# Performance work log

Hardware: AMD Instinct MI355X
Metric: run time of the kernel (lower is better)

The kernel has to match this reference:

```python
import jax, jax.numpy as jnp
import numpy as np

N = 100_000      # nodes
E = 1_600_000    # edges
C_IN = 3         # pos dim
C = 128          # inter_dim == oup_dim
EPS = 1e-5       # BatchNorm eps


def setup_inputs() -> dict:
    key = jax.random.key(0)
    ks = iter(jax.random.split(key, 64))
    inp = {}
    inp['pos'] = jax.random.normal(next(ks), (N, C_IN), dtype=jnp.float32)
    inp['edge_index'] = jax.random.randint(next(ks), (2, E), 0, N, dtype=jnp.int32)
    dims = [C_IN, C, C, C, C]
    for i in range(1, 5):
        cin, cout = dims[i - 1], dims[i]
        inp[f'wl{i}'] = jax.random.normal(next(ks), (cin, cout), jnp.float32) * 0.05
        inp[f'bl{i}'] = jnp.zeros((cout,), jnp.float32)
        inp[f'wr{i}'] = jax.random.normal(next(ks), (cin, cout), jnp.float32) * 0.05
        inp[f'g{i}'] = jax.random.uniform(next(ks), (cout,), jnp.float32, 0.5, 1.5)
        inp[f'be{i}'] = jax.random.normal(next(ks), (cout,), jnp.float32) * 0.1
        inp[f'm{i}'] = jax.random.normal(next(ks), (cout,), jnp.float32) * 0.1
        inp[f'v{i}'] = jax.random.uniform(next(ks), (cout,), jnp.float32, 0.5, 1.5)
    for j, (cin, cout) in enumerate([(C, C), (C, C), (C, C)], start=1):
        inp[f'wf{j}'] = jax.random.normal(next(ks), (cin, cout), jnp.float32) * 0.05
        inp[f'bf{j}'] = jnp.zeros((cout,), jnp.float32)
    return inp


def _sage(x, src, dst, wl, bl, wr):
    # PyG SAGEConv: lin_l(mean_{j->i} x_j) + lin_r(x_i)
    msg_sum = jax.ops.segment_sum(x[src], dst, num_segments=N)          # [N, Cin]
    deg = jax.ops.segment_sum(jnp.ones((src.shape[0], 1), x.dtype), dst, num_segments=N)
    agg = msg_sum / jnp.maximum(deg, 1.0)
    return agg @ wl + bl + x @ wr


def _bn(x, g, b, m, v):
    return g * (x - m) * jax.lax.rsqrt(v + EPS) + b


def reference(pos, edge_index,
              wl1, bl1, wr1, g1, be1, m1, v1,
              wl2, bl2, wr2, g2, be2, m2, v2,
              wl3, bl3, wr3, g3, be3, m3, v3,
              wl4, bl4, wr4, g4, be4, m4, v4,
              wf1, bf1, wf2, bf2, wf3, bf3):
    src, dst = edge_index[0], edge_index[1]
    layers = [(wl1, bl1, wr1, g1, be1, m1, v1),
              (wl2, bl2, wr2, g2, be2, m2, v2),
              (wl3, bl3, wr3, g3, be3, m3, v3),
              (wl4, bl4, wr4, g4, be4, m4, v4)]
    x = pos
    for (wl, bl, wr, g, b, m, v) in layers:
        x = jax.nn.relu(_bn(_sage(x, src, dst, wl, bl, wr), g, b, m, v))
        # dropout p=0.1 inactive at inference
    x = x @ wf1 + bf1
    x = jax.nn.relu(x) @ wf2 + bf2
    x = x @ wf3 + bf3
    return x  # cls=False: raw output, no log_softmax
```

## Files before the change

kernel.cpp:

```cpp
#include <hip/hip_runtime.h>

#define NN 100000
#define EE 1600000
#define CC 128
#define NP 100032
#define NBK 782
#define BCAP 2304

typedef _Float16 f16;
typedef __attribute__((ext_vector_type(2))) f16 f16x2;
typedef __attribute__((ext_vector_type(8))) f16 f16x8;
typedef __attribute__((ext_vector_type(4))) float f32x4;

#define MFMA16(a, b, c) __builtin_amdgcn_mfma_f32_16x16x32_f16(a, b, c, 0, 0, 0)

__global__ __launch_bounds__(1024) void k_part(const int* __restrict__ src,
                                               const int* __restrict__ dst,
                                               int* __restrict__ bcur,
                                               unsigned* __restrict__ bedge) {
  __shared__ int hist[NBK];
  __shared__ int base[NBK];
  const int t = threadIdx.x;
  for (int i = t; i < NBK; i += 1024) hist[i] = 0;
  __syncthreads();
  const int4* src4 = (const int4*)src;
  const int4* dst4 = (const int4*)dst;
  int4 s[4], d[4];
  int rk[16];
  bool val[4];
#pragma unroll
  for (int w = 0; w < 4; w++) {
    int i4 = blockIdx.x * 4096 + w * 1024 + t;
    val[w] = (i4 < EE / 4);
    if (val[w]) {
      s[w] = src4[i4];
      d[w] = dst4[i4];
      rk[w * 4 + 0] = atomicAdd(&hist[d[w].x >> 7], 1);
      rk[w * 4 + 1] = atomicAdd(&hist[d[w].y >> 7], 1);
      rk[w * 4 + 2] = atomicAdd(&hist[d[w].z >> 7], 1);
      rk[w * 4 + 3] = atomicAdd(&hist[d[w].w >> 7], 1);
    }
  }
  __syncthreads();
  for (int i = t; i < NBK; i += 1024) {
    int c = hist[i];
    base[i] = c ? atomicAdd(&bcur[i], c) : 0;
  }
  __syncthreads();
#pragma unroll
  for (int w = 0; w < 4; w++) {
    if (val[w]) {
      int ss[4] = {s[w].x, s[w].y, s[w].z, s[w].w};
      int dd[4] = {d[w].x, d[w].y, d[w].z, d[w].w};
#pragma unroll
      for (int q = 0; q < 4; q++) {
        int b = dd[q] >> 7;
        int slot = base[b] + rk[w * 4 + q];
        if (slot < BCAP)
          bedge[(size_t)b * BCAP + slot] =
              (unsigned)ss[q] | ((unsigned)(dd[q] & 127) << 17);
      }
    }
  }
}

__global__ __launch_bounds__(1024) void k_bscan(const int* __restrict__ bcur,
                                                int* __restrict__ bbase,
                                                int* __restrict__ off) {
  __shared__ int sh[1024];
  int t = threadIdx.x;
  int v = (t < NBK) ? min(bcur[t], BCAP) : 0;
  sh[t] = v;
  __syncthreads();
  for (int d = 1; d < 1024; d <<= 1) {
    int a = (t >= d) ? sh[t - d] : 0;
    __syncthreads();
    sh[t] += a;
    __syncthreads();
  }
  if (t < NBK) bbase[t] = sh[t] - v;
  if (t == 1023) off[NN] = sh[1023];
}

__global__ __launch_bounds__(256) void k_bfill2(const int* __restrict__ bcur,
                                                const int* __restrict__ bbase,
                                                const unsigned* __restrict__ bedge,
                                                int* __restrict__ off,
                                                int* __restrict__ csr) {
  __shared__ int h[128];
  __shared__ int sc[128];
  __shared__ int curs[128];
  const int b = blockIdx.x;
  const int t = threadIdx.x;
  if (t < 128) h[t] = 0;
  __syncthreads();
  const int cnt = min(bcur[b], BCAP);
  const unsigned* be = bedge + (size_t)b * BCAP;
  for (int i = t; i < cnt; i += 256) atomicAdd(&h[(be[i] >> 17) & 127], 1);
  __syncthreads();
  int v = (t < 128) ? h[t] : 0;
  if (t < 128) sc[t] = v;
  __syncthreads();
  for (int d = 1; d < 128; d <<= 1) {
    int a = (t >= d && t < 128) ? sc[t - d] : 0;
    __syncthreads();
    if (t < 128) sc[t] += a;
    __syncthreads();
  }
  if (t < 128) {
    int o = bbase[b] + sc[t] - v;
    int n = b * 128 + t;
    if (n < NN) off[n] = o;
    curs[t] = o;
  }
  __syncthreads();
  for (int i = t; i < cnt; i += 256) {
    unsigned u = be[i];
    int node = (u >> 17) & 127;
    int p = atomicAdd(&curs[node], 1);
    csr[p] = (int)(u & 0x1FFFF);
  }
}

struct WPtrs { const float* w[9]; };
__global__ __launch_bounds__(256) void k_packw(WPtrs wp, f16* __restrict__ out) {
  int t = blockIdx.x * 256 + threadIdx.x;
  int mat = t >> 14;
  int idx = t & 16383;
  int j = idx & 7;
  int lane = (idx >> 3) & 63;
  int ks = (idx >> 9) & 3;
  int nt = idx >> 11;
  int c16 = lane & 15, quad = lane >> 4;
  int k = ks * 32 + quad * 8 + j;
  int n = nt * 16 + c16;
  out[(size_t)mat * 16384 + idx] = (f16)wp.w[mat][k * CC + n];
}

__global__ __launch_bounds__(256) void k_agg3(const int* __restrict__ off,
                                              const int* __restrict__ csr,
                                              const float* __restrict__ pos,
                                              float* __restrict__ agg3) {
  int n = blockIdx.x * 256 + threadIdx.x;
  if (n >= NN) return;
  int b = off[n], e = off[n + 1];
  float a0 = 0.f, a1 = 0.f, a2 = 0.f;
  int i = b;
  for (; i + 4 <= e; i += 4) {
    int s0 = csr[i], s1 = csr[i + 1], s2 = csr[i + 2], s3 = csr[i + 3];
    float p00 = pos[s0 * 3 + 0], p01 = pos[s0 * 3 + 1], p02 = pos[s0 * 3 + 2];
    float p10 = pos[s1 * 3 + 0], p11 = pos[s1 * 3 + 1], p12 = pos[s1 * 3 + 2];
    float p20 = pos[s2 * 3 + 0], p21 = pos[s2 * 3 + 1], p22 = pos[s2 * 3 + 2];
    float p30 = pos[s3 * 3 + 0], p31 = pos[s3 * 3 + 1], p32 = pos[s3 * 3 + 2];
    a0 += (p00 + p10) + (p20 + p30);
    a1 += (p01 + p11) + (p21 + p31);
    a2 += (p02 + p12) + (p22 + p32);
  }
  for (; i < e; i++) {
    int s = csr[i];
    a0 += pos[s * 3 + 0];
    a1 += pos[s * 3 + 1];
    a2 += pos[s * 3 + 2];
  }
  float rd = 1.0f / fmaxf((float)(e - b), 1.0f);
  agg3[n * 3 + 0] = a0 * rd;
  agg3[n * 3 + 1] = a1 * rd;
  agg3[n * 3 + 2] = a2 * rd;
}

__global__ __launch_bounds__(256) void k_node1(
    const float* __restrict__ agg3, const float* __restrict__ pos,
    const float* __restrict__ wl, const float* __restrict__ bl,
    const float* __restrict__ wr, const float* __restrict__ g,
    const float* __restrict__ be, const float* __restrict__ bm,
    const float* __restrict__ bv, f16* __restrict__ x) {
  const int c = threadIdx.x & 127;
  const int np = threadIdx.x >> 7;
  const float Wl0 = wl[c], Wl1 = wl[CC + c], Wl2 = wl[2 * CC + c];
  const float Wr0 = wr[c], Wr1 = wr[CC + c], Wr2 = wr[2 * CC + c];
  const float sc = g[c] * rsqrtf(bv[c] + 1e-5f);
  const float o0 = be[c] + (bl[c] - bm[c]) * sc;
  const int nbase = blockIdx.x * 256;
  const int nend = min(nbase + 256, NN);
#pragma unroll 4
  for (int n = nbase + np; n < nend; n += 2) {
    float acc = agg3[n * 3 + 0] * Wl0 + agg3[n * 3 + 1] * Wl1 +
                agg3[n * 3 + 2] * Wl2 + pos[n * 3 + 0] * Wr0 +
                pos[n * 3 + 1] * Wr1 + pos[n * 3 + 2] * Wr2;
    x[(size_t)n * CC + c] = (f16)fmaxf(acc * sc + o0, 0.0f);
  }
}

__global__ __launch_bounds__(256) void k_aggregate(const int* __restrict__ off,
                                                   const int* __restrict__ csr,
                                                   const f16* __restrict__ x,
                                                   f16* __restrict__ agg) {
  const int n = blockIdx.x * 4 + (threadIdx.x >> 6);
  const int lane = threadIdx.x & 63;
  const int b = off[n], e = off[n + 1];
  float a0 = 0.f, a1 = 0.f;
  int i = b;
  for (; i + 16 <= e; i += 16) {
    int sdx[16];
#pragma unroll
    for (int q = 0; q < 16; q++) sdx[q] = csr[i + q];
    f16x2 v[16];
#pragma unroll
    for (int q = 0; q < 16; q++)
      v[q] = *(const f16x2*)(x + (size_t)sdx[q] * CC + lane * 2);
#pragma unroll
    for (int q = 0; q < 16; q++) {
      a0 += (float)v[q][0];
      a1 += (float)v[q][1];
    }
  }
  const int lim = e - i;
  if (lim > 0) {
    int sdx[16];
#pragma unroll
    for (int q = 0; q < 16; q++) sdx[q] = csr[i + (q < lim ? q : lim - 1)];
    f16x2 v[16];
#pragma unroll
    for (int q = 0; q < 16; q++)
      v[q] = *(const f16x2*)(x + (size_t)sdx[q] * CC + lane * 2);
#pragma unroll
    for (int q = 0; q < 16; q++) {
      if (q < lim) {
        a0 += (float)v[q][0];
        a1 += (float)v[q][1];
      }
    }
  }
  const float rd = 1.0f / fmaxf((float)(e - b), 1.0f);
  f16x2 o;
  o[0] = (f16)(a0 * rd);
  o[1] = (f16)(a1 * rd);
  *(f16x2*)(agg + (size_t)n * CC + lane * 2) = o;
}

__global__ __launch_bounds__(256) void k_sage_mfma(
    const f16* __restrict__ xin, f16* __restrict__ xout,
    const f16* __restrict__ agg, const f16* __restrict__ wl,
    const f16* __restrict__ wr, const float* __restrict__ bl,
    const float* __restrict__ g, const float* __restrict__ be,
    const float* __restrict__ bm, const float* __restrict__ bv) {
  const int lane = threadIdx.x & 63;
  const int wave = threadIdx.x >> 6;
  const int c16 = lane & 15;
  const int quad = lane >> 4;
  const int n0 = blockIdx.x * 64 + wave * 16;
  const int rowX = n0 + c16;
  const int rowA = min(rowX, NN - 1);
  const f16* px = xin + (size_t)rowX * CC + quad * 8;
  const f16* pa = agg + (size_t)rowA * CC + quad * 8;
  f32x4 acc[8];
#pragma unroll
  for (int t = 0; t < 8; t++) acc[t] = {0.f, 0.f, 0.f, 0.f};
#pragma unroll
  for (int ks = 0; ks < 4; ks++) {
    f16x8 Ax = *(const f16x8*)(px + ks * 32);
    f16x8 Aa = *(const f16x8*)(pa + ks * 32);
#pragma unroll
    for (int nt = 0; nt < 8; nt++) {
      const size_t wo = (size_t)((nt * 4 + ks) * 64 + lane) * 8;
      f16x8 Bl = *(const f16x8*)(wl + wo);
      f16x8 Br = *(const f16x8*)(wr + wo);
      acc[nt] = MFMA16(Aa, Bl, acc[nt]);
      acc[nt] = MFMA16(Ax, Br, acc[nt]);
    }
  }
#pragma unroll
  for (int nt = 0; nt < 8; nt++) {
    const int col = nt * 16 + c16;
    const float blc = bl[col];
    const float sc = g[col] * rsqrtf(bv[col] + 1e-5f);
    const float mm = bm[col];
    const float bb = be[col];
#pragma unroll
    for (int r = 0; r < 4; r++) {
      const int node = n0 + quad * 4 + r;
      if (node < NN) {
        float yv = fmaxf((acc[nt][r] + blc - mm) * sc + bb, 0.0f);
        xout[(size_t)node * CC + col] = (f16)yv;
      }
    }
  }
}

__global__ __launch_bounds__(256) void k_dense_fused(
    const f16* __restrict__ x, const f16* __restrict__ w1,
    const f16* __restrict__ w2, const f16* __restrict__ w3,
    const float* __restrict__ b1, const float* __restrict__ b2,
    const float* __restrict__ b3, float* __restrict__ out) {
  const int lane = threadIdx.x & 63;
  const int wave = threadIdx.x >> 6;
  const int c16 = lane & 15;
  const int quad = lane >> 4;
  const int n0 = blockIdx.x * 64 + wave * 16;
  const int lrow = wave * 16;
  __shared__ f16 sh[64][136];

  f32x4 acc[8];
#pragma unroll
  for (int t = 0; t < 8; t++) acc[t] = {0.f, 0.f, 0.f, 0.f};
  const f16* px = x + (size_t)(n0 + c16) * CC + quad * 8;
#pragma unroll
  for (int ks = 0; ks < 4; ks++) {
    f16x8 Ax = *(const f16x8*)(px + ks * 32);
#pragma unroll
    for (int nt = 0; nt < 8; nt++) {
      f16x8 B = *(const f16x8*)(w1 + (size_t)((nt * 4 + ks) * 64 + lane) * 8);
      acc[nt] = MFMA16(Ax, B, acc[nt]);
    }
  }
#pragma unroll
  for (int nt = 0; nt < 8; nt++) {
    const int col = nt * 16 + c16;
    const float bc = b1[col];
#pragma unroll
    for (int r = 0; r < 4; r++)
      sh[lrow + quad * 4 + r][col] = (f16)fmaxf(acc[nt][r] + bc, 0.0f);
  }
#pragma unroll
  for (int t = 0; t < 8; t++) acc[t] = {0.f, 0.f, 0.f, 0.f};
#pragma unroll
  for (int ks = 0; ks < 4; ks++) {
    f16x8 Ax = *(const f16x8*)&sh[lrow + c16][ks * 32 + quad * 8];
#pragma unroll
    for (int nt = 0; nt < 8; nt++) {
      f16x8 B = *(const f16x8*)(w2 + (size_t)((nt * 4 + ks) * 64 + lane) * 8);
      acc[nt] = MFMA16(Ax, B, acc[nt]);
    }
  }
#pragma unroll
  for (int nt = 0; nt < 8; nt++) {
    const int col = nt * 16 + c16;
    const float bc = b2[col];
#pragma unroll
    for (int r = 0; r < 4; r++)
      sh[lrow + quad * 4 + r][col] = (f16)(acc[nt][r] + bc);
  }
#pragma unroll
  for (int t = 0; t < 8; t++) acc[t] = {0.f, 0.f, 0.f, 0.f};
#pragma unroll
  for (int ks = 0; ks < 4; ks++) {
    f16x8 Ax = *(const f16x8*)&sh[lrow + c16][ks * 32 + quad * 8];
#pragma unroll
    for (int nt = 0; nt < 8; nt++) {
      f16x8 B = *(const f16x8*)(w3 + (size_t)((nt * 4 + ks) * 64 + lane) * 8);
      acc[nt] = MFMA16(Ax, B, acc[nt]);
    }
  }
#pragma unroll
  for (int nt = 0; nt < 8; nt++) {
    const int col = nt * 16 + c16;
    const float bc = b3[col];
#pragma unroll
    for (int r = 0; r < 4; r++) {
      const int node = n0 + quad * 4 + r;
      if (node < NN) out[(size_t)node * CC + col] = acc[nt][r] + bc;
    }
  }
}

extern "C" void kernel_launch(void* const* d_in, const int* in_sizes, int n_in,
                              void* d_out, int out_size, void* d_ws,
                              size_t ws_size, hipStream_t stream) {
  const float* pos = (const float*)d_in[0];
  const int* ei = (const int*)d_in[1];
  const int* src = ei;
  const int* dst = ei + EE;
  auto P = [&](int i) { return (const float*)d_in[i]; };

  int* bcur = (int*)d_ws;
  int* bbase = bcur + NBK;
  int* off = bbase + NBK;
  unsigned* bedge = (unsigned*)(off + NN + 2);
  int* csr = (int*)(bedge + (size_t)NBK * BCAP);
  f16* wp16 = (f16*)(csr + EE);
  f16* xa = wp16 + 9 * 16384;
  f16* xb = xa + (size_t)NP * CC;

  f16* agg = (f16*)d_out;

  hipMemsetAsync(bcur, 0, NBK * sizeof(int), stream);

  k_part<<<(EE / 4 + 4095) / 4096, 1024, 0, stream>>>(src, dst, bcur, bedge);
  k_bscan<<<1, 1024, 0, stream>>>(bcur, bbase, off);
  k_bfill2<<<NBK, 256, 0, stream>>>(bcur, bbase, bedge, off, csr);

  WPtrs wp;
  const int wsrc[9] = {9, 11, 16, 18, 23, 25, 30, 32, 34};
  for (int i = 0; i < 9; i++) wp.w[i] = P(wsrc[i]);
  k_packw<<<(9 * 16384) / 256, 256, 0, stream>>>(wp, wp16);

  k_agg3<<<(NN + 255) / 256, 256, 0, stream>>>(off, csr, pos, (float*)d_out);
  k_node1<<<(NN + 255) / 256, 256, 0, stream>>>(
      (const float*)d_out, pos, P(2), P(3), P(4), P(5), P(6), P(7), P(8), xa);

  const int NB = NP / 64;
  const f16* xi = xa;
  f16* xo = xb;
  for (int l = 1; l < 4; l++) {
    int base = 2 + 7 * l;
    int mat = (l - 1) * 2;
    k_aggregate<<<NN / 4, 256, 0, stream>>>(off, csr, xi, agg);
    k_sage_mfma<<<NB, 256, 0, stream>>>(xi, xo, agg,
                                        wp16 + (size_t)mat * 16384,
                                        wp16 + (size_t)(mat + 1) * 16384,
                                        P(base + 1), P(base + 3), P(base + 4),
                                        P(base + 5), P(base + 6));
    const f16* t = xi;
    xi = xo;
    xo = (f16*)t;
  }

  k_dense_fused<<<NB, 256, 0, stream>>>(xi, wp16 + (size_t)6 * 16384,
                                        wp16 + (size_t)7 * 16384,
                                        wp16 + (size_t)8 * 16384, P(31), P(33),
                                        P(35), (float*)d_out);
}
```

Measured before the change: 565.0 us.

## Store node features in channel-slab layout and aggregate per 16-channel slab

Node feature tensors are changed from row-major [N,128] to eight slabs of [NP,16] f16, and all producers and consumers (node1, sage MFMA, dense) are re-indexed to match. Aggregation launches one block group per slab, where each wave handles 16 edges in parallel with 4 lanes per 8-byte row chunk and then reduces across lanes with shuffles. The goal is to make each slab (about 3.2 MB) small enough to stay cache-resident during the random gather, instead of pulling scattered full rows. The cost is eightfold repeated reading of the CSR indices and extra shuffle reductions.

```diff
diff --git a/kernel.cpp b/kernel.cpp
--- a/kernel.cpp
+++ b/kernel.cpp
@@ -9,10 +9,12 @@
 
 typedef _Float16 f16;
 typedef __attribute__((ext_vector_type(2))) f16 f16x2;
+typedef __attribute__((ext_vector_type(4))) f16 f16x4;
 typedef __attribute__((ext_vector_type(8))) f16 f16x8;
 typedef __attribute__((ext_vector_type(4))) float f32x4;
 
 #define MFMA16(a, b, c) __builtin_amdgcn_mfma_f32_16x16x32_f16(a, b, c, 0, 0, 0)
+
 
 __global__ __launch_bounds__(1024) void k_part(const int* __restrict__ src,
                                                const int* __restrict__ dst,
@@ -180,6 +182,7 @@
   const float Wr0 = wr[c], Wr1 = wr[CC + c], Wr2 = wr[2 * CC + c];
   const float sc = g[c] * rsqrtf(bv[c] + 1e-5f);
   const float o0 = be[c] + (bl[c] - bm[c]) * sc;
+  const size_t sb = ((size_t)(c >> 4) * NP) * 16 + (c & 15);
   const int nbase = blockIdx.x * 256;
   const int nend = min(nbase + 256, NN);
 #pragma unroll 4
@@ -187,55 +190,49 @@
     float acc = agg3[n * 3 + 0] * Wl0 + agg3[n * 3 + 1] * Wl1 +
                 agg3[n * 3 + 2] * Wl2 + pos[n * 3 + 0] * Wr0 +
                 pos[n * 3 + 1] * Wr1 + pos[n * 3 + 2] * Wr2;
-    x[(size_t)n * CC + c] = (f16)fmaxf(acc * sc + o0, 0.0f);
-  }
-}
-
-__global__ __launch_bounds__(256) void k_aggregate(const int* __restrict__ off,
-                                                   const int* __restrict__ csr,
-                                                   const f16* __restrict__ x,
-                                                   f16* __restrict__ agg) {
-  const int n = blockIdx.x * 4 + (threadIdx.x >> 6);
+    x[sb + (size_t)n * 16] = (f16)fmaxf(acc * sc + o0, 0.0f);
+  }
+}
+
+__global__ __launch_bounds__(256) void k_agg_slab(const int* __restrict__ off,
+                                                  const int* __restrict__ csr,
+                                                  const f16* __restrict__ x,
+                                                  f16* __restrict__ agg) {
+  const int slab = blockIdx.x & 7;
+  const int n = (blockIdx.x >> 3) * 4 + (threadIdx.x >> 6);
   const int lane = threadIdx.x & 63;
+  const int eg = lane >> 2;
+  const int cl = lane & 3;
   const int b = off[n], e = off[n + 1];
-  float a0 = 0.f, a1 = 0.f;
-  int i = b;
-  for (; i + 16 <= e; i += 16) {
-    int sdx[16];
-#pragma unroll
-    for (int q = 0; q < 16; q++) sdx[q] = csr[i + q];
-    f16x2 v[16];
-#pragma unroll
-    for (int q = 0; q < 16; q++)
-      v[q] = *(const f16x2*)(x + (size_t)sdx[q] * CC + lane * 2);
-#pragma unroll
-    for (int q = 0; q < 16; q++) {
-      a0 += (float)v[q][0];
-      a1 += (float)v[q][1];
-    }
-  }
-  const int lim = e - i;
-  if (lim > 0) {
-    int sdx[16];
-#pragma unroll
-    for (int q = 0; q < 16; q++) sdx[q] = csr[i + (q < lim ? q : lim - 1)];
-    f16x2 v[16];
-#pragma unroll
-    for (int q = 0; q < 16; q++)
-      v[q] = *(const f16x2*)(x + (size_t)sdx[q] * CC + lane * 2);
-#pragma unroll
-    for (int q = 0; q < 16; q++) {
-      if (q < lim) {
-        a0 += (float)v[q][0];
-        a1 += (float)v[q][1];
-      }
-    }
-  }
-  const float rd = 1.0f / fmaxf((float)(e - b), 1.0f);
-  f16x2 o;
-  o[0] = (f16)(a0 * rd);
-  o[1] = (f16)(a1 * rd);
-  *(f16x2*)(agg + (size_t)n * CC + lane * 2) = o;
+  const f16* xs = x + (size_t)slab * NP * 16 + cl * 4;
+  float a0 = 0.f, a1 = 0.f, a2 = 0.f, a3 = 0.f;
+  for (int i = b; i < e; i += 16) {
+    const int j = i + eg;
+    const int idx = csr[min(j, e - 1)];
+    f16x4 v = *(const f16x4*)(xs + (size_t)idx * 16);
+    if (j < e) {
+      a0 += (float)v[0];
+      a1 += (float)v[1];
+      a2 += (float)v[2];
+      a3 += (float)v[3];
+    }
+  }
+#pragma unroll
+  for (int m = 4; m < 64; m <<= 1) {
+    a0 += __shfl_xor(a0, m);
+    a1 += __shfl_xor(a1, m);
+    a2 += __shfl_xor(a2, m);
+    a3 += __shfl_xor(a3, m);
+  }
+  if (lane < 4) {
+    const float rd = 1.0f / fmaxf((float)(e - b), 1.0f);
+    f16x4 o;
+    o[0] = (f16)(a0 * rd);
+    o[1] = (f16)(a1 * rd);
+    o[2] = (f16)(a2 * rd);
+    o[3] = (f16)(a3 * rd);
+    *(f16x4*)(agg + ((size_t)slab * NP + n) * 16 + cl * 4) = o;
+  }
 }
 
 __global__ __launch_bounds__(256) void k_sage_mfma(
@@ -251,15 +248,15 @@
   const int n0 = blockIdx.x * 64 + wave * 16;
   const int rowX = n0 + c16;
   const int rowA = min(rowX, NN - 1);
-  const f16* px = xin + (size_t)rowX * CC + quad * 8;
-  const f16* pa = agg + (size_t)rowA * CC + quad * 8;
   f32x4 acc[8];
 #pragma unroll
   for (int t = 0; t < 8; t++) acc[t] = {0.f, 0.f, 0.f, 0.f};
 #pragma unroll
   for (int ks = 0; ks < 4; ks++) {
-    f16x8 Ax = *(const f16x8*)(px + ks * 32);
-    f16x8 Aa = *(const f16x8*)(pa + ks * 32);
+    const int cb = ks * 32 + quad * 8;
+    const size_t sb = ((size_t)(cb >> 4) * NP) * 16 + (cb & 8);
+    f16x8 Ax = *(const f16x8*)(xin + sb + (size_t)rowX * 16);
+    f16x8 Aa = *(const f16x8*)(agg + sb + (size_t)rowA * 16);
 #pragma unroll
     for (int nt = 0; nt < 8; nt++) {
       const size_t wo = (size_t)((nt * 4 + ks) * 64 + lane) * 8;
@@ -281,7 +278,7 @@
       const int node = n0 + quad * 4 + r;
       if (node < NN) {
         float yv = fmaxf((acc[nt][r] + blc - mm) * sc + bb, 0.0f);
-        xout[(size_t)node * CC + col] = (f16)yv;
+        xout[((size_t)nt * NP + node) * 16 + c16] = (f16)yv;
       }
     }
   }
@@ -303,10 +300,12 @@
   f32x4 acc[8];
 #pragma unroll
   for (int t = 0; t < 8; t++) acc[t] = {0.f, 0.f, 0.f, 0.f};
-  const f16* px = x + (size_t)(n0 + c16) * CC + quad * 8;
+  const int rowX = n0 + c16;
 #pragma unroll
   for (int ks = 0; ks < 4; ks++) {
-    f16x8 Ax = *(const f16x8*)(px + ks * 32);
+    const int cb = ks * 32 + quad * 8;
+    const size_t sb = ((size_t)(cb >> 4) * NP) * 16 + (cb & 8);
+    f16x8 Ax = *(const f16x8*)(x + sb + (size_t)rowX * 16);
 #pragma unroll
     for (int nt = 0; nt < 8; nt++) {
       f16x8 B = *(const f16x8*)(w1 + (size_t)((nt * 4 + ks) * 64 + lane) * 8);
@@ -404,7 +403,7 @@
   for (int l = 1; l < 4; l++) {
     int base = 2 + 7 * l;
     int mat = (l - 1) * 2;
-    k_aggregate<<<NN / 4, 256, 0, stream>>>(off, csr, xi, agg);
+    k_agg_slab<<<(NN / 4) * 8, 256, 0, stream>>>(off, csr, xi, agg);
     k_sage_mfma<<<NB, 256, 0, stream>>>(xi, xo, agg,
                                         wp16 + (size_t)mat * 16384,
                                         wp16 + (size_t)(mat + 1) * 16384,
```

Result: slower. 879.0 us (+55.6%).

## Fuse neighbor mean aggregation into SAGE MFMA kernel via shared memory

Applied to the files above, without the earlier changes.

Merges the per-layer gather/mean aggregation kernel with the MFMA linear+BN+ReLU kernel. Each wave aggregates its 16 rows into an LDS tile, then reads the aggregated A operand from shared memory instead of global. This removes the global round trip of the aggregated features and one launch per layer. In exchange, each wave now walks its 16 nodes serially, and the grid drops from 25000 to about 1563 blocks, which lowers parallelism and memory-level concurrency in the latency-bound gather.

```diff
diff --git a/kernel.cpp b/kernel.cpp
--- a/kernel.cpp
+++ b/kernel.cpp
@@ -13,6 +13,7 @@
 typedef __attribute__((ext_vector_type(4))) float f32x4;
 
 #define MFMA16(a, b, c) __builtin_amdgcn_mfma_f32_16x16x32_f16(a, b, c, 0, 0, 0)
+
 
 __global__ __launch_bounds__(1024) void k_part(const int* __restrict__ src,
                                                const int* __restrict__ dst,
@@ -191,75 +192,77 @@
   }
 }
 
-__global__ __launch_bounds__(256) void k_aggregate(const int* __restrict__ off,
-                                                   const int* __restrict__ csr,
-                                                   const f16* __restrict__ x,
-                                                   f16* __restrict__ agg) {
-  const int n = blockIdx.x * 4 + (threadIdx.x >> 6);
-  const int lane = threadIdx.x & 63;
-  const int b = off[n], e = off[n + 1];
-  float a0 = 0.f, a1 = 0.f;
-  int i = b;
-  for (; i + 16 <= e; i += 16) {
-    int sdx[16];
-#pragma unroll
-    for (int q = 0; q < 16; q++) sdx[q] = csr[i + q];
-    f16x2 v[16];
-#pragma unroll
-    for (int q = 0; q < 16; q++)
-      v[q] = *(const f16x2*)(x + (size_t)sdx[q] * CC + lane * 2);
-#pragma unroll
-    for (int q = 0; q < 16; q++) {
-      a0 += (float)v[q][0];
-      a1 += (float)v[q][1];
-    }
-  }
-  const int lim = e - i;
-  if (lim > 0) {
-    int sdx[16];
-#pragma unroll
-    for (int q = 0; q < 16; q++) sdx[q] = csr[i + (q < lim ? q : lim - 1)];
-    f16x2 v[16];
-#pragma unroll
-    for (int q = 0; q < 16; q++)
-      v[q] = *(const f16x2*)(x + (size_t)sdx[q] * CC + lane * 2);
-#pragma unroll
-    for (int q = 0; q < 16; q++) {
-      if (q < lim) {
-        a0 += (float)v[q][0];
-        a1 += (float)v[q][1];
-      }
-    }
-  }
-  const float rd = 1.0f / fmaxf((float)(e - b), 1.0f);
-  f16x2 o;
-  o[0] = (f16)(a0 * rd);
-  o[1] = (f16)(a1 * rd);
-  *(f16x2*)(agg + (size_t)n * CC + lane * 2) = o;
-}
-
-__global__ __launch_bounds__(256) void k_sage_mfma(
+__global__ __launch_bounds__(256) void k_agg_sage(
+    const int* __restrict__ off, const int* __restrict__ csr,
     const f16* __restrict__ xin, f16* __restrict__ xout,
-    const f16* __restrict__ agg, const f16* __restrict__ wl,
-    const f16* __restrict__ wr, const float* __restrict__ bl,
-    const float* __restrict__ g, const float* __restrict__ be,
-    const float* __restrict__ bm, const float* __restrict__ bv) {
+    const f16* __restrict__ wl, const f16* __restrict__ wr,
+    const float* __restrict__ bl, const float* __restrict__ g,
+    const float* __restrict__ be, const float* __restrict__ bm,
+    const float* __restrict__ bv) {
   const int lane = threadIdx.x & 63;
   const int wave = threadIdx.x >> 6;
   const int c16 = lane & 15;
   const int quad = lane >> 4;
   const int n0 = blockIdx.x * 64 + wave * 16;
+  const int lrow = wave * 16;
+  __shared__ f16 sh[64][136];
+
+  for (int k = 0; k < 16; k++) {
+    const int n = n0 + k;
+    float a0 = 0.f, a1 = 0.f;
+    if (n < NN) {
+      const int b = off[n], e = off[n + 1];
+      int i = b;
+      for (; i + 16 <= e; i += 16) {
+        int sdx[16];
+#pragma unroll
+        for (int q = 0; q < 16; q++) sdx[q] = csr[i + q];
+        f16x2 v[16];
+#pragma unroll
+        for (int q = 0; q < 16; q++)
+          v[q] = *(const f16x2*)(xin + (size_t)sdx[q] * CC + lane * 2);
+#pragma unroll
+        for (int q = 0; q < 16; q++) {
+          a0 += (float)v[q][0];
+          a1 += (float)v[q][1];
+        }
+      }
+      const int lim = e - i;
+      if (lim > 0) {
+        int sdx[16];
+#pragma unroll
+        for (int q = 0; q < 16; q++) sdx[q] = csr[i + (q < lim ? q : lim - 1)];
+        f16x2 v[16];
+#pragma unroll
+        for (int q = 0; q < 16; q++)
+          v[q] = *(const f16x2*)(xin + (size_t)sdx[q] * CC + lane * 2);
+#pragma unroll
+        for (int q = 0; q < 16; q++) {
+          if (q < lim) {
+            a0 += (float)v[q][0];
+            a1 += (float)v[q][1];
+          }
+        }
+      }
+      const float rd = 1.0f / fmaxf((float)(e - b), 1.0f);
+      a0 *= rd;
+      a1 *= rd;
+    }
+    f16x2 o;
+    o[0] = (f16)a0;
+    o[1] = (f16)a1;
+    *(f16x2*)&sh[lrow + k][lane * 2] = o;
+  }
+
   const int rowX = n0 + c16;
-  const int rowA = min(rowX, NN - 1);
   const f16* px = xin + (size_t)rowX * CC + quad * 8;
-  const f16* pa = agg + (size_t)rowA * CC + quad * 8;
   f32x4 acc[8];
 #pragma unroll
   for (int t = 0; t < 8; t++) acc[t] = {0.f, 0.f, 0.f, 0.f};
 #pragma unroll
   for (int ks = 0; ks < 4; ks++) {
     f16x8 Ax = *(const f16x8*)(px + ks * 32);
-    f16x8 Aa = *(const f16x8*)(pa + ks * 32);
+    f16x8 Aa = *(const f16x8*)&sh[lrow + c16][ks * 32 + quad * 8];
 #pragma unroll
     for (int nt = 0; nt < 8; nt++) {
       const size_t wo = (size_t)((nt * 4 + ks) * 64 + lane) * 8;
@@ -381,8 +384,6 @@
   f16* xa = wp16 + 9 * 16384;
   f16* xb = xa + (size_t)NP * CC;
 
-  f16* agg = (f16*)d_out;
-
   hipMemsetAsync(bcur, 0, NBK * sizeof(int), stream);
 
   k_part<<<(EE / 4 + 4095) / 4096, 1024, 0, stream>>>(src, dst, bcur, bedge);
@@ -404,12 +405,11 @@
   for (int l = 1; l < 4; l++) {
     int base = 2 + 7 * l;
     int mat = (l - 1) * 2;
-    k_aggregate<<<NN / 4, 256, 0, stream>>>(off, csr, xi, agg);
-    k_sage_mfma<<<NB, 256, 0, stream>>>(xi, xo, agg,
-                                        wp16 + (size_t)mat * 16384,
-                                        wp16 + (size_t)(mat + 1) * 16384,
-                                        P(base + 1), P(base + 3), P(base + 4),
-                                        P(base + 5), P(base + 6));
+    k_agg_sage<<<NB, 256, 0, stream>>>(off, csr, xi, xo,
+                                       wp16 + (size_t)mat * 16384,
+                                       wp16 + (size_t)(mat + 1) * 16384,
+                                       P(base + 1), P(base + 3), P(base + 4),
+                                       P(base + 5), P(base + 6));
     const f16* t = xi;
     xi = xo;
     xo = (f16*)t;
```

Result: no change. 568.5 us (+0.6%).
